# Performance work log

Measured on AMD Instinct MI355X. Metric: run time of the kernel, lower is better.

## Reference

```python
import jax, jax.numpy as jnp
import numpy as np

B, S, D, H, L, FF, V, TYPES = 16, 512, 1024, 16, 8, 4096, 30522, 2
DH = D // H
BETA = 1.0          # pbit_temperature
EPS = 1e-12         # layer_norm_eps
STD = 0.02          # initializer_range


def _ln(x, g, b):
    m = x.mean(-1, keepdims=True)
    v = ((x - m) ** 2).mean(-1, keepdims=True)
    return (x - m) * jax.lax.rsqrt(v + EPS) * g + b


def setup_inputs() -> dict:
    key = jax.random.key(0)
    ks = iter(jax.random.split(key, 32))
    rn = lambda shape: (jax.random.normal(next(ks), shape, dtype=jnp.float32) * STD)
    inp = {
        'input_ids': jax.random.randint(next(ks), (B, S), 0, V),
        'token_type_ids': jax.random.randint(next(ks), (B, S), 0, TYPES),
        'tok_emb': rn((V, D)),
        'pos_emb': rn((S, D)),
        'type_emb': rn((TYPES, D)),
        'emb_g': jnp.ones((D,), jnp.float32),
        'emb_b': jnp.zeros((D,), jnp.float32),
        # stacked per-layer parameters [L, ...]
        'Wq': rn((L, D, D)), 'bq': jnp.zeros((L, D), jnp.float32),
        'Wk': rn((L, D, D)), 'bk': jnp.zeros((L, D), jnp.float32),
        'Wv': rn((L, D, D)), 'bv': jnp.zeros((L, D), jnp.float32),
        'Wo': rn((L, D, D)), 'bo': jnp.zeros((L, D), jnp.float32),
        'ln1_g': jnp.ones((L, D), jnp.float32), 'ln1_b': jnp.zeros((L, D), jnp.float32),
        'ln2_g': jnp.ones((L, D), jnp.float32), 'ln2_b': jnp.zeros((L, D), jnp.float32),
        'W1': rn((L, D, FF)), 'b1': jnp.zeros((L, FF), jnp.float32),
        'W2': rn((L, FF, D)), 'b2': jnp.zeros((L, D), jnp.float32),
    }
    return inp


def reference(input_ids, token_type_ids, tok_emb, pos_emb, type_emb, emb_g, emb_b,
              Wq, bq, Wk, bk, Wv, bv, Wo, bo, ln1_g, ln1_b, ln2_g, ln2_b,
              W1, b1, W2, b2):
    # Embeddings (eval mode: TSU noise + dropout are identity)
    h = tok_emb[input_ids] + pos_emb[None, :, :] + type_emb[token_type_ids]
    h = _ln(h, emb_g, emb_b)

    def layer(h, p):
        wq, bq_, wk, bk_, wv, bv_, wo, bo_, g1, bb1, g2, bb2, w1, bf1, w2, bf2 = p
        x = _ln(h, g1, bb1)  # pre-LN per TinyBioBERTLayer
        q = (x @ wq + bq_).reshape(B, S, H, DH)
        k = (x @ wk + bk_).reshape(B, S, H, DH)
        v = (x @ wv + bv_).reshape(B, S, H, DH)
        # P-bit attention in expectation == temperature-scaled softmax SDPA
        scores = jnp.einsum('bqhd,bkhd->bhqk', q, k) * (BETA / np.sqrt(DH))
        a = jax.nn.softmax(scores, axis=-1)
        ctx = jnp.einsum('bhqk,bkhd->bqhd', a, v).reshape(B, S, D)
        h = h + ctx @ wo + bo_
        y = _ln(h, g2, bb2)
        y = jax.nn.gelu(y @ w1 + bf1, approximate=False) @ w2 + bf2
        return h + y, None

    params = (Wq, bq, Wk, bk, Wv, bv, Wo, bo, ln1_g, ln1_b, ln2_g, ln2_b, W1, b1, W2, b2)
    h, _ = jax.lax.scan(layer, h, params)
    return h
```

## Files before the change

### kernel.cpp

```cpp
#include <hip/hip_runtime.h>
#include <math.h>

#define B_  16
#define S_  512
#define D_  1024
#define H_  16
#define DH_ 64
#define L_  8
#define FF_ 4096
#define M_  (B_*S_)

typedef __attribute__((ext_vector_type(4))) float  f32x4;
typedef __attribute__((ext_vector_type(8))) short  s8v;
typedef __attribute__((ext_vector_type(4))) short  s4v;
typedef __attribute__((ext_vector_type(8))) __bf16 bf8v;

__device__ __forceinline__ short f2bf(float f) {
  union { float f; unsigned u; } x; x.f = f;
  unsigned r = x.u + 0x7fffu + ((x.u >> 16) & 1u);
  return (short)(r >> 16);
}

__device__ __forceinline__ f32x4 mfma16(s8v a, s8v b, f32x4 c) {
  return __builtin_amdgcn_mfma_f32_16x16x32_bf16(
      __builtin_bit_cast(bf8v, a), __builtin_bit_cast(bf8v, b), c, 0, 0, 0);
}

__device__ __forceinline__ void gl_lds16(const void* g, void* lds) {
  __builtin_amdgcn_global_load_lds(
      (const __attribute__((address_space(1))) unsigned int*)g,
      (__attribute__((address_space(3))) unsigned int*)lds, 16, 0, 0);
}

__device__ __forceinline__ float gelu_exact(float v) {
  return 0.5f * v * (1.0f + erff(v * 0.70710678118654752f));
}

__global__ __launch_bounds__(256) void tcvt(const float* __restrict__ src,
                                            short* __restrict__ dst, int R, int C,
                                            size_t dls) {
  __shared__ float tile[32][33];
  src += (size_t)blockIdx.z * R * C;
  dst += (size_t)blockIdx.z * dls;
  const int c0 = blockIdx.x * 32, r0 = blockIdx.y * 32;
  const int tx = threadIdx.x & 31, ty = threadIdx.x >> 5;
#pragma unroll
  for (int i = 0; i < 32; i += 8)
    tile[ty + i][tx] = src[(size_t)(r0 + ty + i) * C + (c0 + tx)];
  __syncthreads();
#pragma unroll
  for (int i = 0; i < 32; i += 8)
    dst[(size_t)(c0 + ty + i) * R + (r0 + tx)] = f2bf(tile[tx][ty + i]);
}

__global__ __launch_bounds__(256) void embed_ln(
    const int* __restrict__ ids, const int* __restrict__ tts,
    const float* __restrict__ tok, const float* __restrict__ pos,
    const float* __restrict__ typ, const float* __restrict__ g,
    const float* __restrict__ bta, float* __restrict__ h) {
  const int row = blockIdx.x;
  const int s = row & (S_ - 1);
  const int id = ids[row], tt = tts[row];
  const int t = threadIdx.x;
  const float4 a = ((const float4*)(tok + (size_t)id * D_))[t];
  const float4 p = ((const float4*)(pos + (size_t)s  * D_))[t];
  const float4 y = ((const float4*)(typ + (size_t)tt * D_))[t];
  float x0 = a.x + p.x + y.x, x1 = a.y + p.y + y.y;
  float x2 = a.z + p.z + y.z, x3 = a.w + p.w + y.w;
  float sum = x0 + x1 + x2 + x3;
  float sq  = x0*x0 + x1*x1 + x2*x2 + x3*x3;
  __shared__ float red[8];
#pragma unroll
  for (int d = 1; d < 64; d <<= 1) { sum += __shfl_xor(sum, d); sq += __shfl_xor(sq, d); }
  if ((t & 63) == 0) { red[t >> 6] = sum; red[(t >> 6) + 4] = sq; }
  __syncthreads();
  sum = red[0] + red[1] + red[2] + red[3];
  sq  = red[4] + red[5] + red[6] + red[7];
  const float mean = sum * (1.f / D_);
  const float var  = sq * (1.f / D_) - mean * mean;
  const float rstd = rsqrtf(fmaxf(var, 0.f) + 1e-12f);
  const float4 gg = ((const float4*)g)[t];
  const float4 bb = ((const float4*)bta)[t];
  float4 o;
  o.x = (x0 - mean) * rstd * gg.x + bb.x;
  o.y = (x1 - mean) * rstd * gg.y + bb.y;
  o.z = (x2 - mean) * rstd * gg.z + bb.z;
  o.w = (x3 - mean) * rstd * gg.w + bb.w;
  ((float4*)(h + (size_t)row * D_))[t] = o;
}

__global__ __launch_bounds__(256) void ln_bf16(
    const float* __restrict__ h, const float* __restrict__ g,
    const float* __restrict__ bta, short* __restrict__ out) {
  const int row = blockIdx.x;
  const int t = threadIdx.x;
  const float4 x = ((const float4*)(h + (size_t)row * D_))[t];
  float sum = x.x + x.y + x.z + x.w;
  float sq  = x.x*x.x + x.y*x.y + x.z*x.z + x.w*x.w;
  __shared__ float red[8];
#pragma unroll
  for (int d = 1; d < 64; d <<= 1) { sum += __shfl_xor(sum, d); sq += __shfl_xor(sq, d); }
  if ((t & 63) == 0) { red[t >> 6] = sum; red[(t >> 6) + 4] = sq; }
  __syncthreads();
  sum = red[0] + red[1] + red[2] + red[3];
  sq  = red[4] + red[5] + red[6] + red[7];
  const float mean = sum * (1.f / D_);
  const float var  = sq * (1.f / D_) - mean * mean;
  const float rstd = rsqrtf(fmaxf(var, 0.f) + 1e-12f);
  const float4 gg = ((const float4*)g)[t];
  const float4 bb = ((const float4*)bta)[t];
  s4v o;
  o[0] = f2bf((x.x - mean) * rstd * gg.x + bb.x);
  o[1] = f2bf((x.y - mean) * rstd * gg.y + bb.y);
  o[2] = f2bf((x.z - mean) * rstd * gg.z + bb.z);
  o[3] = f2bf((x.w - mean) * rstd * gg.w + bb.w);
  *(s4v*)&out[(size_t)row * D_ + t * 4] = o;
}

template<int MODE>
__global__ __launch_bounds__(256, 2) void gemm_bt(
    const short* __restrict__ A, const short* __restrict__ Bt,
    const float* __restrict__ b0, const float* __restrict__ b1,
    const float* __restrict__ b2, short* __restrict__ out,
    float* __restrict__ hres, int N, int K) {
  __shared__ __align__(16) short As[128 * 32];
  __shared__ __align__(16) short Bs[128 * 32];
  const int tid = threadIdx.x;
  const int wid = tid >> 6, lane = tid & 63;
  const int wr = wid >> 1, wc = wid & 1;
  const int l15 = lane & 15, l4 = lane >> 4;

  const short* Ab = A + (size_t)blockIdx.x * 128 * K;
  const short* Bb = Bt + (size_t)blockIdx.y * 128 * K;

  const f32x4 zero4 = {0.f, 0.f, 0.f, 0.f};
  f32x4 acc[4][4];
#pragma unroll
  for (int i = 0; i < 4; ++i)
#pragma unroll
    for (int j = 0; j < 4; ++j) acc[i][j] = zero4;

  const int ldrow = lane >> 2;
  const int ldcol = (lane & 3) * 8;

  for (int k0 = 0; k0 < K; k0 += 32) {
#pragma unroll
    for (int c = 0; c < 2; ++c) {
      const int seg = wid * 2 + c;
      gl_lds16(Ab + (size_t)(seg * 16 + ldrow) * K + (k0 + ldcol), (char*)As + seg * 1024);
      gl_lds16(Bb + (size_t)(seg * 16 + ldrow) * K + (k0 + ldcol), (char*)Bs + seg * 1024);
    }
    __syncthreads();
    s8v af[4], bf[4];
#pragma unroll
    for (int mf = 0; mf < 4; ++mf)
      af[mf] = *(const s8v*)&As[(wr * 64 + mf * 16 + l15) * 32 + l4 * 8];
#pragma unroll
    for (int nf = 0; nf < 4; ++nf)
      bf[nf] = *(const s8v*)&Bs[(wc * 64 + nf * 16 + l15) * 32 + l4 * 8];
#pragma unroll
    for (int mf = 0; mf < 4; ++mf)
#pragma unroll
      for (int nf = 0; nf < 4; ++nf)
        acc[mf][nf] = mfma16(af[mf], bf[nf], acc[mf][nf]);
    __syncthreads();
  }

  const int r0 = blockIdx.x * 128 + wr * 64;
  const int c0 = blockIdx.y * 128 + wc * 64;
  const int which = c0 >> 10;
  const float* bias = (MODE == 3) ? (which == 0 ? b0 : (which == 1 ? b1 : b2)) : b0;
  short* out3 = (MODE == 3) ? out + (size_t)which * M_ * D_ : out;

#pragma unroll
  for (int mf = 0; mf < 4; ++mf) {
#pragma unroll
    for (int nf = 0; nf < 4; ++nf) {
      const int col = c0 + nf * 16 + l15;
      const int colw = col & (D_ - 1);
      const float bb = bias[MODE == 3 ? colw : col];
#pragma unroll
      for (int r = 0; r < 4; ++r) {
        const int row = r0 + mf * 16 + l4 * 4 + r;
        const float v = acc[mf][nf][r] + bb;
        if (MODE == 0) {
          out[(size_t)row * N + col] = f2bf(v);
        } else if (MODE == 1) {
          out[(size_t)row * N + col] = f2bf(gelu_exact(v));
        } else if (MODE == 2) {
          hres[(size_t)row * N + col] += v;
        } else {
          const int b = row >> 9, s = row & 511, hd = colw >> 6, dh = colw & 63;
          out3[((((size_t)b * H_ + hd) * S_ + s) << 6) + dh] = f2bf(v);
        }
      }
    }
  }
}

__global__ __launch_bounds__(256, 2) void attn(
    const short* __restrict__ Q, const short* __restrict__ K,
    const short* __restrict__ V, short* __restrict__ ctx) {
  __shared__ __align__(16) short Kl[32][72];
  __shared__ __align__(16) short Vt[DH_][40];
  __shared__ __align__(16) short Pl[4][32 * 40];

  const int tid = threadIdx.x, wid = tid >> 6, lane = tid & 63;
  const int l15 = lane & 15, l4 = lane >> 4;
  const int bh = blockIdx.y;
  const size_t base = (size_t)bh * S_ * DH_;
  const short* Qb = Q + base;
  const short* Kb = K + base;
  const short* Vb = V + base;

  const int qoff = blockIdx.x * 128 + wid * 32;

  s8v qf[2][2];
#pragma unroll
  for (int mf = 0; mf < 2; ++mf)
#pragma unroll
    for (int ks = 0; ks < 2; ++ks)
      qf[mf][ks] = *(const s8v*)&Qb[(size_t)(qoff + mf * 16 + l15) * DH_ + ks * 32 + l4 * 8];

  const f32x4 zero4 = {0.f, 0.f, 0.f, 0.f};
  f32x4 o[2][4];
  float rm[2][4], rs[2][4];
#pragma unroll
  for (int mf = 0; mf < 2; ++mf) {
#pragma unroll
    for (int nf = 0; nf < 4; ++nf) o[mf][nf] = zero4;
#pragma unroll
    for (int r = 0; r < 4; ++r) { rm[mf][r] = -1e30f; rs[mf][r] = 0.f; }
  }

  const int str = tid >> 3;
  const int stc = (tid & 7) * 8;

  for (int kt = 0; kt < S_ / 32; ++kt) {
    __syncthreads();
    {
      const s8v kk = *(const s8v*)&Kb[(size_t)(kt * 32 + str) * DH_ + stc];
      *(s8v*)&Kl[str][stc] = kk;
      const s8v vv = *(const s8v*)&Vb[(size_t)(kt * 32 + str) * DH_ + stc];
#pragma unroll
      for (int j = 0; j < 8; ++j) Vt[stc + j][str] = vv[j];
    }
    __syncthreads();

    f32x4 sc[2][2];
#pragma unroll
    for (int mf = 0; mf < 2; ++mf)
#pragma unroll
      for (int nt = 0; nt < 2; ++nt) sc[mf][nt] = zero4;
#pragma unroll
    for (int nt = 0; nt < 2; ++nt)
#pragma unroll
      for (int ks = 0; ks < 2; ++ks) {
        const s8v kf = *(const s8v*)&Kl[nt * 16 + l15][ks * 32 + l4 * 8];
#pragma unroll
        for (int mf = 0; mf < 2; ++mf)
          sc[mf][nt] = mfma16(qf[mf][ks], kf, sc[mf][nt]);
      }

#pragma unroll
    for (int mf = 0; mf < 2; ++mf) {
      float tm[4];
#pragma unroll
      for (int r = 0; r < 4; ++r) {
        sc[mf][0][r] *= 0.125f; sc[mf][1][r] *= 0.125f;
        tm[r] = fmaxf(sc[mf][0][r], sc[mf][1][r]);
      }
#pragma unroll
      for (int d = 1; d < 16; d <<= 1)
#pragma unroll
        for (int r = 0; r < 4; ++r) tm[r] = fmaxf(tm[r], __shfl_xor(tm[r], d));
      float ps[4];
#pragma unroll
      for (int r = 0; r < 4; ++r) {
        const float nm = fmaxf(rm[mf][r], tm[r]);
        const float so = __expf(rm[mf][r] - nm);
        rm[mf][r] = nm;
        rs[mf][r] *= so;
#pragma unroll
        for (int nf = 0; nf < 4; ++nf) o[mf][nf][r] *= so;
        const float p0 = __expf(sc[mf][0][r] - nm);
        const float p1 = __expf(sc[mf][1][r] - nm);
        sc[mf][0][r] = p0; sc[mf][1][r] = p1;
        ps[r] = p0 + p1;
      }
#pragma unroll
      for (int d = 1; d < 16; d <<= 1)
#pragma unroll
        for (int r = 0; r < 4; ++r) ps[r] += __shfl_xor(ps[r], d);
#pragma unroll
      for (int r = 0; r < 4; ++r) rs[mf][r] += ps[r];
#pragma unroll
      for (int nt = 0; nt < 2; ++nt)
#pragma unroll
        for (int r = 0; r < 4; ++r)
          Pl[wid][(mf * 16 + l4 * 4 + r) * 40 + nt * 16 + l15] = f2bf(sc[mf][nt][r]);
    }
    asm volatile("s_waitcnt lgkmcnt(0)" ::: "memory");

    s8v vf[4];
#pragma unroll
    for (int nf = 0; nf < 4; ++nf)
      vf[nf] = *(const s8v*)&Vt[nf * 16 + l15][l4 * 8];
#pragma unroll
    for (int mf = 0; mf < 2; ++mf) {
      const s8v pf = *(const s8v*)&Pl[wid][(mf * 16 + l15) * 40 + l4 * 8];
#pragma unroll
      for (int nf = 0; nf < 4; ++nf)
        o[mf][nf] = mfma16(pf, vf[nf], o[mf][nf]);
    }
  }

  const int bb = bh >> 4, hh = bh & 15;
#pragma unroll
  for (int mf = 0; mf < 2; ++mf)
#pragma unroll
    for (int r = 0; r < 4; ++r) {
      const int qrow = qoff + mf * 16 + l4 * 4 + r;
      const float inv = 1.0f / rs[mf][r];
      short* dst = ctx + (size_t)(bb * S_ + qrow) * D_ + hh * DH_;
#pragma unroll
      for (int nf = 0; nf < 4; ++nf)
        dst[nf * 16 + l15] = f2bf(o[mf][nf][r] * inv);
    }
}

extern "C" void kernel_launch(void* const* d_in, const int* in_sizes, int n_in,
                              void* d_out, int out_size, void* d_ws, size_t ws_size,
                              hipStream_t stream) {
  const int*   ids = (const int*)d_in[0];
  const int*   tts = (const int*)d_in[1];
  const float* tok = (const float*)d_in[2];
  const float* pos = (const float*)d_in[3];
  const float* typ = (const float*)d_in[4];
  const float* eg  = (const float*)d_in[5];
  const float* eb  = (const float*)d_in[6];
  const float* Wq  = (const float*)d_in[7];  const float* bq = (const float*)d_in[8];
  const float* Wk  = (const float*)d_in[9];  const float* bk = (const float*)d_in[10];
  const float* Wv  = (const float*)d_in[11]; const float* bv = (const float*)d_in[12];
  const float* Wo  = (const float*)d_in[13]; const float* bo = (const float*)d_in[14];
  const float* g1  = (const float*)d_in[15]; const float* be1 = (const float*)d_in[16];
  const float* g2  = (const float*)d_in[17]; const float* be2 = (const float*)d_in[18];
  const float* W1  = (const float*)d_in[19]; const float* b1 = (const float*)d_in[20];
  const float* W2  = (const float*)d_in[21]; const float* b2 = (const float*)d_in[22];

  float* h = (float*)d_out;

  const size_t szDD  = (size_t)D_ * D_;
  const size_t szDF  = (size_t)D_ * FF_;
  const size_t xb_b  = (size_t)M_ * D_ * 2;
  const size_t big_b = (size_t)M_ * FF_ * 2;
  const size_t wfull = (szDD * 4 + szDF * 2) * 2 * L_;
  const bool full = ws_size >= wfull + xb_b + big_b + 8192;

  char* p = (char*)d_ws;
  auto alloc = [&](size_t bytes) { char* r = p; p += (bytes + 255) & ~(size_t)255; return r; };
  const size_t wl = full ? L_ : 1;
  short* wqkvT = (short*)alloc(szDD * 3 * 2 * wl);
  short* woT   = (short*)alloc(szDD * 2 * wl);
  short* w1T   = (short*)alloc(szDF * 2 * wl);
  short* w2T   = (short*)alloc(szDF * 2 * wl);
  short* xb  = (short*)alloc(xb_b);
  char*  big = alloc(big_b);
  short* qb  = (short*)big;
  short* cb  = xb;
  short* tb  = (short*)big;

  if (full) {
    tcvt<<<dim3(D_/32,  D_/32,  L_), 256, 0, stream>>>(Wq, wqkvT,            D_,  D_,  3*szDD);
    tcvt<<<dim3(D_/32,  D_/32,  L_), 256, 0, stream>>>(Wk, wqkvT +   szDD,   D_,  D_,  3*szDD);
    tcvt<<<dim3(D_/32,  D_/32,  L_), 256, 0, stream>>>(Wv, wqkvT + 2*szDD,   D_,  D_,  3*szDD);
    tcvt<<<dim3(D_/32,  D_/32,  L_), 256, 0, stream>>>(Wo, woT, D_,  D_,  szDD);
    tcvt<<<dim3(FF_/32, D_/32,  L_), 256, 0, stream>>>(W1, w1T, D_,  FF_, szDF);
    tcvt<<<dim3(D_/32,  FF_/32, L_), 256, 0, stream>>>(W2, w2T, FF_, D_,  szDF);
  }

  embed_ln<<<M_, 256, 0, stream>>>(ids, tts, tok, pos, typ, eg, eb, h);

  for (int l = 0; l < L_; ++l) {
    if (!full) {
      tcvt<<<dim3(D_/32,  D_/32,  1), 256, 0, stream>>>(Wq + (size_t)l*szDD, wqkvT,          D_,  D_,  0);
      tcvt<<<dim3(D_/32,  D_/32,  1), 256, 0, stream>>>(Wk + (size_t)l*szDD, wqkvT +   szDD, D_,  D_,  0);
      tcvt<<<dim3(D_/32,  D_/32,  1), 256, 0, stream>>>(Wv + (size_t)l*szDD, wqkvT + 2*szDD, D_,  D_,  0);
      tcvt<<<dim3(D_/32,  D_/32,  1), 256, 0, stream>>>(Wo + (size_t)l*szDD, woT, D_,  D_,  0);
      tcvt<<<dim3(FF_/32, D_/32,  1), 256, 0, stream>>>(W1 + (size_t)l*szDF, w1T, D_,  FF_, 0);
      tcvt<<<dim3(D_/32,  FF_/32, 1), 256, 0, stream>>>(W2 + (size_t)l*szDF, w2T, FF_, D_,  0);
    }
    const size_t o3 = full ? (size_t)l * 3 * szDD : 0;
    const size_t od = full ? (size_t)l * szDD : 0;
    const size_t of = full ? (size_t)l * szDF : 0;

    ln_bf16<<<M_, 256, 0, stream>>>(h, g1 + l*D_, be1 + l*D_, xb);
    gemm_bt<3><<<dim3(M_/128, 3*D_/128), 256, 0, stream>>>(
        xb, wqkvT + o3, bq + l*D_, bk + l*D_, bv + l*D_, qb, nullptr, D_, D_);
    attn<<<dim3(S_/128, B_*H_), 256, 0, stream>>>(qb, qb + (size_t)M_*D_, qb + 2*(size_t)M_*D_, cb);
    gemm_bt<2><<<dim3(M_/128, D_/128), 256, 0, stream>>>(
        cb, woT + od, bo + l*D_, nullptr, nullptr, nullptr, h, D_, D_);
    ln_bf16<<<M_, 256, 0, stream>>>(h, g2 + l*D_, be2 + l*D_, xb);
    gemm_bt<1><<<dim3(M_/128, FF_/128), 256, 0, stream>>>(
        xb, w1T + of, b1 + l*FF_, nullptr, nullptr, tb, nullptr, FF_, D_);
    gemm_bt<2><<<dim3(M_/128, D_/128), 256, 0, stream>>>(
        tb, w2T + of, b2 + l*D_, nullptr, nullptr, nullptr, h, D_, FF_);
  }
}
```

Measured before the change: 3.746 ms.

## Replace GEMM with 256x256 tile, 8-wave, double-buffered pipelined MFMA kernel

The 128x128 single-buffered GEMM is replaced by a 512-thread kernel that computes 256x256 tiles with a K-step of 64. It double-buffers 128KB of LDS using direct global-to-LDS loads, applies an XOR swizzle against bank conflicts, and interleaves loads with MFMA phases under explicit waitcnt, barriers and setprio. Blocks are remapped so that groups of 8 share tiles, for better L2 locality. The goal is more data reuse per LDS byte and loads overlapped with compute, at the cost of 128KB LDS per block and much higher register pressure, which lowers occupancy.

```diff
diff --git a/kernel.cpp b/kernel.cpp
--- a/kernel.cpp
+++ b/kernel.cpp
@@ -118,84 +118,135 @@
 }
 
 template<int MODE>
-__global__ __launch_bounds__(256, 2) void gemm_bt(
+__global__ __launch_bounds__(512, 2) void gemm8(
     const short* __restrict__ A, const short* __restrict__ Bt,
     const float* __restrict__ b0, const float* __restrict__ b1,
     const float* __restrict__ b2, short* __restrict__ out,
-    float* __restrict__ hres, int N, int K) {
-  __shared__ __align__(16) short As[128 * 32];
-  __shared__ __align__(16) short Bs[128 * 32];
-  const int tid = threadIdx.x;
-  const int wid = tid >> 6, lane = tid & 63;
-  const int wr = wid >> 1, wc = wid & 1;
+    float* __restrict__ hres, int N, int K, int nbx) {
+  __shared__ __align__(16) char lds[131072];
+  const int tid = threadIdx.x, wid = tid >> 6, lane = tid & 63;
+  const int wr = wid >> 2, wc = wid & 3;
   const int l15 = lane & 15, l4 = lane >> 4;
 
-  const short* Ab = A + (size_t)blockIdx.x * 128 * K;
-  const short* Bb = Bt + (size_t)blockIdx.y * 128 * K;
-
-  const f32x4 zero4 = {0.f, 0.f, 0.f, 0.f};
-  f32x4 acc[4][4];
-#pragma unroll
-  for (int i = 0; i < 4; ++i)
-#pragma unroll
-    for (int j = 0; j < 4; ++j) acc[i][j] = zero4;
-
-  const int ldrow = lane >> 2;
-  const int ldcol = (lane & 3) * 8;
-
-  for (int k0 = 0; k0 < K; k0 += 32) {
-#pragma unroll
-    for (int c = 0; c < 2; ++c) {
-      const int seg = wid * 2 + c;
-      gl_lds16(Ab + (size_t)(seg * 16 + ldrow) * K + (k0 + ldcol), (char*)As + seg * 1024);
-      gl_lds16(Bb + (size_t)(seg * 16 + ldrow) * K + (k0 + ldcol), (char*)Bs + seg * 1024);
-    }
-    __syncthreads();
-    s8v af[4], bf[4];
-#pragma unroll
-    for (int mf = 0; mf < 4; ++mf)
-      af[mf] = *(const s8v*)&As[(wr * 64 + mf * 16 + l15) * 32 + l4 * 8];
-#pragma unroll
-    for (int nf = 0; nf < 4; ++nf)
-      bf[nf] = *(const s8v*)&Bs[(wc * 64 + nf * 16 + l15) * 32 + l4 * 8];
-#pragma unroll
-    for (int mf = 0; mf < 4; ++mf)
-#pragma unroll
-      for (int nf = 0; nf < 4; ++nf)
-        acc[mf][nf] = mfma16(af[mf], bf[nf], acc[mf][nf]);
-    __syncthreads();
-  }
-
-  const int r0 = blockIdx.x * 128 + wr * 64;
-  const int c0 = blockIdx.y * 128 + wc * 64;
-  const int which = c0 >> 10;
-  const float* bias = (MODE == 3) ? (which == 0 ? b0 : (which == 1 ? b1 : b2)) : b0;
-  short* out3 = (MODE == 3) ? out + (size_t)which * M_ * D_ : out;
-
-#pragma unroll
-  for (int mf = 0; mf < 4; ++mf) {
-#pragma unroll
-    for (int nf = 0; nf < 4; ++nf) {
-      const int col = c0 + nf * 16 + l15;
-      const int colw = col & (D_ - 1);
-      const float bb = bias[MODE == 3 ? colw : col];
-#pragma unroll
-      for (int r = 0; r < 4; ++r) {
-        const int row = r0 + mf * 16 + l4 * 4 + r;
-        const float v = acc[mf][nf][r] + bb;
-        if (MODE == 0) {
-          out[(size_t)row * N + col] = f2bf(v);
-        } else if (MODE == 1) {
-          out[(size_t)row * N + col] = f2bf(gelu_exact(v));
-        } else if (MODE == 2) {
-          hres[(size_t)row * N + col] += v;
-        } else {
+  const int n8 = (int)gridDim.x >> 3;
+  const int bid = (int)blockIdx.x;
+  const int sid = (bid & 7) * n8 + (bid >> 3);
+  const int bx = sid % nbx, by = sid / nbx;
+
+  const short* __restrict__ Ab = A + (size_t)bx * 256 * K;
+  const short* __restrict__ Bb = Bt + (size_t)by * 256 * K;
+
+  const int stc  = ((tid & 7) ^ (((tid >> 5) & 1) << 1)) * 8;
+  const int str0 = tid >> 3;
+  const int kx   = (l4 * 16) ^ (((l15 >> 2) & 1) << 5);
+  const int arow = (wr * 128 + l15) * 128;
+  const int brow = (wc * 64 + l15) * 128;
+
+  f32x4 acc[8][4];
+#pragma unroll
+  for (int m = 0; m < 8; ++m)
+#pragma unroll
+    for (int n = 0; n < 4; ++n) acc[m][n] = f32x4{0.f, 0.f, 0.f, 0.f};
+  s8v af[8][2], bf[4][2];
+
+  const int nt = K >> 6, it = nt >> 1;
+
+#define SB_  __builtin_amdgcn_sched_barrier(0)
+#define BAR_ do { SB_; __builtin_amdgcn_s_barrier(); SB_; } while (0)
+#define LGKM0_ do { asm volatile("s_waitcnt lgkmcnt(0)" ::: "memory"); SB_; } while (0)
+#define VMC_(n) do { asm volatile("s_waitcnt vmcnt(" #n ")" ::: "memory"); SB_; } while (0)
+#define ST_(isB, slot, hh, kt) do { \
+    const short* _g = ((isB) ? Bb : Ab) + (size_t)((hh) * 128 + str0) * K + ((kt) << 6) + stc; \
+    char* _d = lds + ((isB) ? 65536 : 0) + (slot) * 32768 + (hh) * 16384 + wid * 1024; \
+    gl_lds16(_g, _d); \
+    gl_lds16(_g + (size_t)64 * K, _d + 8192); \
+  } while (0)
+#define RDA_(slot) do { \
+    const char* _p = lds + (slot) * 32768 + arow + kx; \
+    _Pragma("unroll") for (int _m = 0; _m < 8; ++_m) { \
+      af[_m][0] = *(const s8v*)(_p + _m * 2048); \
+      af[_m][1] = *(const s8v*)(_p + _m * 2048 + 64); } \
+  } while (0)
+#define RDB_(slot, n0, n1) do { \
+    const char* _p = lds + 65536 + (slot) * 32768 + brow + kx; \
+    _Pragma("unroll") for (int _n = (n0); _n <= (n1); ++_n) { \
+      bf[_n][0] = *(const s8v*)(_p + _n * 2048); \
+      bf[_n][1] = *(const s8v*)(_p + _n * 2048 + 64); } \
+  } while (0)
+#define MM_(mq, nq) do { \
+    __builtin_amdgcn_s_setprio(1); \
+    _Pragma("unroll") for (int _mf = 0; _mf < 4; ++_mf) \
+    _Pragma("unroll") for (int _nf = 0; _nf < 2; ++_nf) \
+    _Pragma("unroll") for (int _ks = 0; _ks < 2; ++_ks) \
+      acc[(mq)*4+_mf][(nq)*2+_nf] = \
+        mfma16(af[(mq)*4+_mf][_ks], bf[(nq)*2+_nf][_ks], acc[(mq)*4+_mf][(nq)*2+_nf]); \
+    __builtin_amdgcn_s_setprio(0); \
+  } while (0)
+
+  ST_(0,0,0,0); ST_(0,0,1,0); ST_(1,0,0,0); ST_(1,0,1,0);
+  ST_(0,1,0,1); ST_(0,1,1,1); ST_(1,1,0,1);
+  VMC_(6);
+  BAR_;
+
+  for (int t = 0; t < it; ++t) {
+    const int ka = 2 * t, kb = ka + 1;
+    const bool s2 = (ka + 2) < nt, s3 = (kb + 2) < nt;
+    RDA_(0); RDB_(0, 0, 1);
+    ST_(1, 1, 1, kb);
+    BAR_; LGKM0_; MM_(0, 0); BAR_;
+    RDB_(0, 2, 3);
+    if (s2) ST_(0, 0, 0, ka + 2);
+    BAR_; LGKM0_; MM_(0, 1); BAR_;
+    if (s2) ST_(0, 0, 1, ka + 2);
+    BAR_; MM_(1, 0); BAR_;
+    if (s2) { ST_(1, 0, 0, ka + 2); VMC_(6); } else { VMC_(0); }
+    BAR_; MM_(1, 1); BAR_;
+    RDA_(1); RDB_(1, 0, 1);
+    if (s2) ST_(1, 0, 1, ka + 2);
+    BAR_; LGKM0_; MM_(0, 0); BAR_;
+    RDB_(1, 2, 3);
+    if (s3) ST_(0, 1, 0, kb + 2);
+    BAR_; LGKM0_; MM_(0, 1); BAR_;
+    if (s3) ST_(0, 1, 1, kb + 2);
+    BAR_; MM_(1, 0); BAR_;
+    if (s3) { ST_(1, 1, 0, kb + 2); VMC_(6); }
+    BAR_; MM_(1, 1); BAR_;
+  }
+
+  const int r0 = bx * 256 + wr * 128;
+  const int c0 = by * 256 + wc * 64;
+  const int which = (MODE == 3) ? (c0 >> 10) : 0;
+  const float* __restrict__ bias =
+      (MODE == 3) ? (which == 0 ? b0 : (which == 1 ? b1 : b2)) : b0;
+  short* __restrict__ outw = (MODE == 3) ? out + (size_t)which * M_ * D_ : out;
+#pragma unroll
+  for (int n = 0; n < 4; ++n) {
+    const int col  = c0 + n * 16 + l15;
+    const int colw = col & (D_ - 1);
+    const float bb = bias[(MODE == 3) ? colw : col];
+#pragma unroll
+    for (int m = 0; m < 8; ++m) {
+#pragma unroll
+      for (int rr = 0; rr < 4; ++rr) {
+        const int row = r0 + m * 16 + l4 * 4 + rr;
+        const float v = acc[m][n][rr] + bb;
+        if (MODE == 1)      outw[(size_t)row * N + col] = f2bf(gelu_exact(v));
+        else if (MODE == 2) hres[(size_t)row * N + col] += v;
+        else if (MODE == 3) {
           const int b = row >> 9, s = row & 511, hd = colw >> 6, dh = colw & 63;
-          out3[((((size_t)b * H_ + hd) * S_ + s) << 6) + dh] = f2bf(v);
-        }
+          outw[((((size_t)b * H_ + hd) * S_ + s) << 6) + dh] = f2bf(v);
+        } else              outw[(size_t)row * N + col] = f2bf(v);
       }
     }
   }
+#undef SB_
+#undef BAR_
+#undef LGKM0_
+#undef VMC_
+#undef ST_
+#undef RDA_
+#undef RDB_
+#undef MM_
 }
 
 __global__ __launch_bounds__(256, 2) void attn(
@@ -371,9 +422,9 @@
   short* tb  = (short*)big;
 
   if (full) {
-    tcvt<<<dim3(D_/32,  D_/32,  L_), 256, 0, stream>>>(Wq, wqkvT,            D_,  D_,  3*szDD);
-    tcvt<<<dim3(D_/32,  D_/32,  L_), 256, 0, stream>>>(Wk, wqkvT +   szDD,   D_,  D_,  3*szDD);
-    tcvt<<<dim3(D_/32,  D_/32,  L_), 256, 0, stream>>>(Wv, wqkvT + 2*szDD,   D_,  D_,  3*szDD);
+    tcvt<<<dim3(D_/32,  D_/32,  L_), 256, 0, stream>>>(Wq, wqkvT,          D_,  D_,  3*szDD);
+    tcvt<<<dim3(D_/32,  D_/32,  L_), 256, 0, stream>>>(Wk, wqkvT +   szDD, D_,  D_,  3*szDD);
+    tcvt<<<dim3(D_/32,  D_/32,  L_), 256, 0, stream>>>(Wv, wqkvT + 2*szDD, D_,  D_,  3*szDD);
     tcvt<<<dim3(D_/32,  D_/32,  L_), 256, 0, stream>>>(Wo, woT, D_,  D_,  szDD);
     tcvt<<<dim3(FF_/32, D_/32,  L_), 256, 0, stream>>>(W1, w1T, D_,  FF_, szDF);
     tcvt<<<dim3(D_/32,  FF_/32, L_), 256, 0, stream>>>(W2, w2T, FF_, D_,  szDF);
@@ -381,6 +432,7 @@
 
   embed_ln<<<M_, 256, 0, stream>>>(ids, tts, tok, pos, typ, eg, eb, h);
 
+  const int nbx = M_ / 256;
   for (int l = 0; l < L_; ++l) {
     if (!full) {
       tcvt<<<dim3(D_/32,  D_/32,  1), 256, 0, stream>>>(Wq + (size_t)l*szDD, wqkvT,          D_,  D_,  0);
@@ -395,15 +447,16 @@
     const size_t of = full ? (size_t)l * szDF : 0;
 
     ln_bf16<<<M_, 256, 0, stream>>>(h, g1 + l*D_, be1 + l*D_, xb);
-    gemm_bt<3><<<dim3(M_/128, 3*D_/128), 256, 0, stream>>>(
-        xb, wqkvT + o3, bq + l*D_, bk + l*D_, bv + l*D_, qb, nullptr, D_, D_);
-    attn<<<dim3(S_/128, B_*H_), 256, 0, stream>>>(qb, qb + (size_t)M_*D_, qb + 2*(size_t)M_*D_, cb);
-    gemm_bt<2><<<dim3(M_/128, D_/128), 256, 0, stream>>>(
-        cb, woT + od, bo + l*D_, nullptr, nullptr, nullptr, h, D_, D_);
+    gemm8<3><<<nbx * (3*D_/256), 512, 0, stream>>>(
+        xb, wqkvT + o3, bq + l*D_, bk + l*D_, bv + l*D_, qb, nullptr, 3*D_, D_, nbx);
+    attn<<<dim3(S_/128, B_*H_), 256, 0, stream>>>(
+        qb, qb + (size_t)M_*D_, qb + 2*(size_t)M_*D_, cb);
+    gemm8<2><<<nbx * (D_/256), 512, 0, stream>>>(
+        cb, woT + od, bo + l*D_, nullptr, nullptr, nullptr, h, D_, D_, nbx);
     ln_bf16<<<M_, 256, 0, stream>>>(h, g2 + l*D_, be2 + l*D_, xb);
-    gemm_bt<1><<<dim3(M_/128, FF_/128), 256, 0, stream>>>(
-        xb, w1T + of, b1 + l*FF_, nullptr, nullptr, tb, nullptr, FF_, D_);
-    gemm_bt<2><<<dim3(M_/128, D_/128), 256, 0, stream>>>(
-        tb, w2T + of, b2 + l*D_, nullptr, nullptr, nullptr, h, D_, FF_);
-  }
-}
+    gemm8<1><<<nbx * (FF_/256), 512, 0, stream>>>(
+        xb, w1T + of, b1 + l*FF_, nullptr, nullptr, tb, nullptr, FF_, D_, nbx);
+    gemm8<2><<<nbx * (D_/256), 512, 0, stream>>>(
+        tb, w2T + of, b2 + l*D_, nullptr, nullptr, nullptr, h, D_, FF_, nbx);
+  }
+}
```

Result: slower. 4.147 ms (+10.7%).
